# Kernel optimization log

Measured on AMD Instinct MI355X. Metric: run time of the kernel, lower is better.

The kernel has to match this reference:

```python
import jax, jax.numpy as jnp
import numpy as np

N = 131072   # total nodes
E = 262144   # directed edges (avg degree 2, molecular graphs)
G = 4096     # number of graphs in the batch
H = 64       # hidden_dim


def _linear_init(key, fan_in, fan_out):
    # torch.nn.Linear default: U(-1/sqrt(fan_in), 1/sqrt(fan_in))
    s = 1.0 / np.sqrt(fan_in)
    kw, kb = jax.random.split(key)
    W = jax.random.uniform(kw, (fan_in, fan_out), jnp.float32, -s, s)
    b = jax.random.uniform(kb, (fan_out,), jnp.float32, -s, s)
    return W, b


def setup_inputs() -> dict:
    key = jax.random.key(0)
    ks = jax.random.split(key, 8)
    d = {}
    d["x"] = jax.random.normal(ks[0], (N, 1), jnp.float32)
    d["edge_index"] = jax.random.randint(ks[1], (2, E), 0, N, jnp.int32)
    d["batch"] = jnp.sort(jax.random.randint(ks[2], (N,), 0, G, jnp.int32))
    d["W1"], d["b1"] = _linear_init(ks[3], 1, H)          # GCNConv(1, 64)
    d["W2"], d["b2"] = _linear_init(ks[4], H, 2 * H)       # GCNConv(64, 128)
    d["W3"], d["b3"] = _linear_init(ks[5], 2 * H, 4 * H)   # GCNConv(128, 256)
    d["fc1_W"], d["fc1_b"] = _linear_init(ks[6], 4 * H, 128)
    d["fc2_W"], d["fc2_b"] = _linear_init(ks[7], 128, 12)
    return d


def gcn_conv(x, W, b, src, dst):
    """PyG GCNConv: D^-1/2 (A + I) D^-1/2 (x W) + b, self-loops added."""
    h = x @ W                                                   # [N, out]
    deg = jax.ops.segment_sum(jnp.ones(E, jnp.float32), dst, num_segments=N) + 1.0
    dinv = jax.lax.rsqrt(deg)                                   # [N]
    coef = dinv[src] * dinv[dst]                                # [E]
    agg = jax.ops.segment_sum(h[src] * coef[:, None], dst, num_segments=N)
    agg = agg + h * (dinv * dinv)[:, None]                      # self-loop term: h_i / deg_i
    return agg + b


def reference(x, edge_index, batch, W1, b1, W2, b2, W3, b3, fc1_W, fc1_b, fc2_W, fc2_b):
    src, dst = edge_index[0], edge_index[1]
    h = jax.nn.relu(gcn_conv(x, W1, b1, src, dst))
    h = jax.nn.relu(gcn_conv(h, W2, b2, src, dst))
    h = gcn_conv(h, W3, b3, src, dst)                            # [N, 256]
    # global_mean_pool over batch ids
    sums = jax.ops.segment_sum(h, batch, num_segments=G)         # [G, 256]
    cnts = jax.ops.segment_sum(jnp.ones(N, jnp.float32), batch, num_segments=G)
    g = sums / jnp.maximum(cnts, 1.0)[:, None]
    g = jax.nn.relu(g @ fc1_W + fc1_b)
    return g @ fc2_W + fc2_b                                     # [G, 12]
```

## Files before the change

kernel.cpp:

```cpp
#include <hip/hip_runtime.h>

#define NN 131072
#define EE 262144
#define GG 4096

__global__ void k_count(const int* __restrict__ dst, int* __restrict__ indeg) {
    int e = blockIdx.x * 256 + threadIdx.x;
    if (e < EE) atomicAdd(&indeg[dst[e]], 1);
}

__global__ __launch_bounds__(256) void k_scan_a(const int* __restrict__ indeg,
                                                int* __restrict__ bsum,
                                                float* __restrict__ dinv) {
    __shared__ int red[256];
    int tid = threadIdx.x;
    int gid = blockIdx.x * 256 + tid;
    int v = indeg[gid];
    dinv[gid] = rsqrtf((float)v + 1.0f);
    red[tid] = v;
    __syncthreads();
#pragma unroll
    for (int off = 128; off > 0; off >>= 1) {
        if (tid < off) red[tid] += red[tid + off];
        __syncthreads();
    }
    if (tid == 0) bsum[blockIdx.x] = red[0];
}

__global__ __launch_bounds__(512) void k_scan_b(const int* __restrict__ bsum,
                                                int* __restrict__ boff) {
    __shared__ int ps[512];
    int tid = threadIdx.x;
    ps[tid] = bsum[tid];
    __syncthreads();
    for (int off = 1; off < 512; off <<= 1) {
        int v = (tid >= off) ? ps[tid - off] : 0;
        __syncthreads();
        ps[tid] += v;
        __syncthreads();
    }
    boff[tid] = (tid > 0) ? ps[tid - 1] : 0;
    if (tid == 511) boff[512] = ps[511];
}

__global__ __launch_bounds__(256) void k_scan_c(const int* __restrict__ indeg,
                                                const int* __restrict__ boff,
                                                int* __restrict__ rowptr,
                                                int* __restrict__ cursor) {
    __shared__ int ps[256];
    int tid = threadIdx.x;
    int gid = blockIdx.x * 256 + tid;
    int v = indeg[gid];
    ps[tid] = v;
    __syncthreads();
    for (int off = 1; off < 256; off <<= 1) {
        int t = (tid >= off) ? ps[tid - off] : 0;
        __syncthreads();
        ps[tid] += t;
        __syncthreads();
    }
    int excl = boff[blockIdx.x] + ps[tid] - v;
    rowptr[gid] = excl;
    cursor[gid] = excl;
    if (gid == NN - 1) rowptr[NN] = boff[512];
}

__global__ void k_fill_edges(const int* __restrict__ src, const int* __restrict__ dst,
                             const float* __restrict__ dinv,
                             int* __restrict__ cursor, int* __restrict__ ecol,
                             float* __restrict__ ecoef) {
    int e = blockIdx.x * 256 + threadIdx.x;
    if (e < EE) {
        int d = dst[e], s = src[e];
        int slot = atomicAdd(&cursor[d], 1);
        ecol[slot] = s;
        ecoef[slot] = dinv[d] * dinv[s];
    }
}

__global__ void k_z(const float* __restrict__ x, const float* __restrict__ dinv,
                    const int* __restrict__ rowptr, const int* __restrict__ ecol,
                    const float* __restrict__ ecoef, float* __restrict__ z) {
    int i = blockIdx.x * 256 + threadIdx.x;
    if (i < NN) {
        float di = dinv[i];
        float s = x[i] * di * di;
        int e0 = rowptr[i], e1 = rowptr[i + 1];
        for (int e = e0; e < e1; ++e) s += ecoef[e] * x[ecol[e]];
        z[i] = s;
    }
}

__global__ __launch_bounds__(256) void k_gemm2u(const float* __restrict__ z,
                                                const float* __restrict__ dinv,
                                                const int* __restrict__ rowptr,
                                                const int* __restrict__ ecol,
                                                const float* __restrict__ ecoef,
                                                const float* __restrict__ W1,
                                                const float* __restrict__ b1,
                                                const float* __restrict__ W2,
                                                const float* __restrict__ b2,
                                                float* __restrict__ r) {
    __shared__ float At[64][68];
    __shared__ float Wt[64][128];
    __shared__ float w1s[64], b1s[64];

    int tid = threadIdx.x;
    int i0 = blockIdx.x * 64;

    if (tid < 64) { w1s[tid] = W1[tid]; b1s[tid] = b1[tid]; }
    {
        int c4 = tid & 31, kk0 = tid >> 5;
#pragma unroll
        for (int p = 0; p < 8; ++p) {
            int kk = kk0 + p * 8;
            *(float4*)&Wt[kk][c4 * 4] = *(const float4*)&W2[(size_t)kk * 128 + c4 * 4];
        }
    }
    __syncthreads();

    {
        int n = tid >> 2;
        int k0 = (tid & 3) * 16;
        int i = i0 + n;
        float zi = z[i], di = dinv[i];
        float d2 = di * di;
        float uacc[16];
#pragma unroll
        for (int j = 0; j < 16; ++j)
            uacc[j] = d2 * fmaxf(zi * w1s[k0 + j] + b1s[k0 + j], 0.f);
        int e0 = rowptr[i], e1 = rowptr[i + 1];
        for (int e = e0; e < e1; ++e) {
            float w = ecoef[e];
            float zs = z[ecol[e]];
#pragma unroll
            for (int j = 0; j < 16; ++j)
                uacc[j] += w * fmaxf(zs * w1s[k0 + j] + b1s[k0 + j], 0.f);
        }
#pragma unroll
        for (int j = 0; j < 16; ++j) At[n][k0 + j] = uacc[j];
    }
    __syncthreads();

    int colg = tid & 15;
    int rowg = tid >> 4;
    float acc[4][8];
#pragma unroll
    for (int rr = 0; rr < 4; ++rr)
#pragma unroll
        for (int c = 0; c < 8; ++c) acc[rr][c] = 0.0f;

#pragma unroll 4
    for (int kk = 0; kk < 64; ++kk) {
        float a[4];
#pragma unroll
        for (int rr = 0; rr < 4; ++rr) a[rr] = At[rowg * 4 + rr][kk];
        const float4 w0 = *(const float4*)&Wt[kk][colg * 4];
        const float4 w1 = *(const float4*)&Wt[kk][64 + colg * 4];
        float w[8] = {w0.x, w0.y, w0.z, w0.w, w1.x, w1.y, w1.z, w1.w};
#pragma unroll
        for (int rr = 0; rr < 4; ++rr)
#pragma unroll
            for (int c = 0; c < 8; ++c) acc[rr][c] += a[rr] * w[c];
    }

#pragma unroll
    for (int rr = 0; rr < 4; ++rr) {
        int i = i0 + rowg * 4 + rr;
#pragma unroll
        for (int h = 0; h < 2; ++h) {
            int j = h * 64 + colg * 4;
            const float4 b = *(const float4*)&b2[j];
            float4 v;
            v.x = fmaxf(acc[rr][h * 4 + 0] + b.x, 0.f);
            v.y = fmaxf(acc[rr][h * 4 + 1] + b.y, 0.f);
            v.z = fmaxf(acc[rr][h * 4 + 2] + b.z, 0.f);
            v.w = fmaxf(acc[rr][h * 4 + 3] + b.w, 0.f);
            *(float4*)&r[(size_t)i * 128 + j] = v;
        }
    }
}

template <int K, int OUTW, bool RELU_OUT, bool GUARD>
__global__ __launch_bounds__(256) void k_gemm(const float* __restrict__ A,
                                              const float* __restrict__ W,
                                              const float* __restrict__ bias,
                                              const float* __restrict__ cntf,
                                              float* __restrict__ C) {
    __shared__ float At[64][68];
    __shared__ float Wt[64][128];

    int tid  = threadIdx.x;
    int colg = tid & 15;
    int rowg = tid >> 4;
    int i0 = blockIdx.x * 64;
    int j0 = blockIdx.y * 128;

    float acc[4][8];
#pragma unroll
    for (int r = 0; r < 4; ++r)
#pragma unroll
        for (int c = 0; c < 8; ++c) acc[r][c] = 0.0f;

    for (int k0 = 0; k0 < K; k0 += 64) {
        __syncthreads();
        {
            int k4 = tid & 15, r0 = tid >> 4;
#pragma unroll
            for (int p = 0; p < 4; ++p) {
                int r = r0 + p * 16;
                *(float4*)&At[r][k4 * 4] =
                    *(const float4*)&A[(size_t)(i0 + r) * K + k0 + k4 * 4];
            }
        }
        {
            int c4 = tid & 31, kk0 = tid >> 5;
#pragma unroll
            for (int p = 0; p < 8; ++p) {
                int kk = kk0 + p * 8;
                *(float4*)&Wt[kk][c4 * 4] =
                    *(const float4*)&W[(size_t)(k0 + kk) * OUTW + j0 + c4 * 4];
            }
        }
        __syncthreads();
#pragma unroll 4
        for (int kk = 0; kk < 64; ++kk) {
            float a[4];
#pragma unroll
            for (int r = 0; r < 4; ++r) a[r] = At[rowg * 4 + r][kk];
            const float4 w0 = *(const float4*)&Wt[kk][colg * 4];
            const float4 w1 = *(const float4*)&Wt[kk][64 + colg * 4];
            float w[8] = {w0.x, w0.y, w0.z, w0.w, w1.x, w1.y, w1.z, w1.w};
#pragma unroll
            for (int r = 0; r < 4; ++r)
#pragma unroll
                for (int c = 0; c < 8; ++c) acc[r][c] += a[r] * w[c];
        }
    }

#pragma unroll
    for (int r = 0; r < 4; ++r) {
        int i = i0 + rowg * 4 + r;
        float flag = 1.0f;
        if (GUARD) flag = (cntf[i] > 0.0f) ? 1.0f : 0.0f;
#pragma unroll
        for (int h = 0; h < 2; ++h) {
            int j = j0 + h * 64 + colg * 4;
            const float4 b = *(const float4*)&bias[j];
            float4 v;
            v.x = acc[r][h * 4 + 0] + b.x * flag;
            v.y = acc[r][h * 4 + 1] + b.y * flag;
            v.z = acc[r][h * 4 + 2] + b.z * flag;
            v.w = acc[r][h * 4 + 3] + b.w * flag;
            if (RELU_OUT) {
                v.x = fmaxf(v.x, 0.f); v.y = fmaxf(v.y, 0.f);
                v.z = fmaxf(v.z, 0.f); v.w = fmaxf(v.w, 0.f);
            }
            *(float4*)&C[(size_t)i * OUTW + j] = v;
        }
    }
}

__global__ __launch_bounds__(256) void k_fc12(const float* __restrict__ A,
                                              const float* __restrict__ W,
                                              const float* __restrict__ bias,
                                              const float* __restrict__ fc2W,
                                              const float* __restrict__ fc2b,
                                              float* __restrict__ out) {
    __shared__ float At[64][68];
    __shared__ float Wt[64][128];

    int tid  = threadIdx.x;
    int colg = tid & 15;
    int rowg = tid >> 4;
    int i0 = blockIdx.x * 64;

    float acc[4][8];
#pragma unroll
    for (int r = 0; r < 4; ++r)
#pragma unroll
        for (int c = 0; c < 8; ++c) acc[r][c] = 0.0f;

    for (int k0 = 0; k0 < 256; k0 += 64) {
        __syncthreads();
        {
            int k4 = tid & 15, r0 = tid >> 4;
#pragma unroll
            for (int p = 0; p < 4; ++p) {
                int r = r0 + p * 16;
                *(float4*)&At[r][k4 * 4] =
                    *(const float4*)&A[(size_t)(i0 + r) * 256 + k0 + k4 * 4];
            }
        }
        {
            int c4 = tid & 31, kk0 = tid >> 5;
#pragma unroll
            for (int p = 0; p < 8; ++p) {
                int kk = kk0 + p * 8;
                *(float4*)&Wt[kk][c4 * 4] =
                    *(const float4*)&W[(size_t)(k0 + kk) * 128 + c4 * 4];
            }
        }
        __syncthreads();
#pragma unroll 4
        for (int kk = 0; kk < 64; ++kk) {
            float a[4];
#pragma unroll
            for (int r = 0; r < 4; ++r) a[r] = At[rowg * 4 + r][kk];
            const float4 w0 = *(const float4*)&Wt[kk][colg * 4];
            const float4 w1 = *(const float4*)&Wt[kk][64 + colg * 4];
            float w[8] = {w0.x, w0.y, w0.z, w0.w, w1.x, w1.y, w1.z, w1.w};
#pragma unroll
            for (int r = 0; r < 4; ++r)
#pragma unroll
                for (int c = 0; c < 8; ++c) acc[r][c] += a[r] * w[c];
        }
    }
    __syncthreads();
    float* g1s = &Wt[0][0];
    float* w2s = &At[0][0];
    for (int idx = tid; idx < 128 * 12; idx += 256) w2s[idx] = fc2W[idx];

#pragma unroll
    for (int r = 0; r < 4; ++r) {
        int row = rowg * 4 + r;
#pragma unroll
        for (int h = 0; h < 2; ++h) {
            int j = h * 64 + colg * 4;
            const float4 b = *(const float4*)&bias[j];
            float4 v;
            v.x = fmaxf(acc[r][h * 4 + 0] + b.x, 0.f);
            v.y = fmaxf(acc[r][h * 4 + 1] + b.y, 0.f);
            v.z = fmaxf(acc[r][h * 4 + 2] + b.z, 0.f);
            v.w = fmaxf(acc[r][h * 4 + 3] + b.w, 0.f);
            *(float4*)&g1s[row * 128 + j] = v;
        }
    }
    __syncthreads();
    for (int idx = tid; idx < 64 * 12; idx += 256) {
        int row = idx / 12, col = idx % 12;
        float o = fc2b[col];
        const float* gr = &g1s[row * 128];
        for (int k = 0; k < 128; ++k) o += gr[k] * w2s[k * 12 + col];
        out[(size_t)(i0 + row) * 12 + col] = o;
    }
}

__global__ __launch_bounds__(256) void k_pool(const float* __restrict__ r,
                                              const float* __restrict__ dinv,
                                              const int* __restrict__ rowptr,
                                              const int* __restrict__ ecol,
                                              const float* __restrict__ ecoef,
                                              const int* __restrict__ batch,
                                              float* __restrict__ Y,
                                              float* __restrict__ cntf) {
    int g = blockIdx.x, tid = threadIdx.x;
    int l = 0, rr = NN;
    while (l < rr) { int m = (l + rr) >> 1; if (batch[m] < g) l = m + 1; else rr = m; }
    int lo = l;
    rr = NN;
    while (l < rr) { int m = (l + rr) >> 1; if (batch[m] < g + 1) l = m + 1; else rr = m; }
    int hi = l;
    int cnt = hi - lo;

    int lane = tid & 31, ty = tid >> 5;
    int c = lane * 4;
    float4 acc = {0.f, 0.f, 0.f, 0.f};

    int i = lo + ty;
    for (; i + 8 < hi; i += 16) {
        float d0 = dinv[i], d1 = dinv[i + 8];
        const float4 v0 = *(const float4*)&r[(size_t)i * 128 + c];
        const float4 v1 = *(const float4*)&r[(size_t)(i + 8) * 128 + c];
        float w0 = d0 * d0, w1 = d1 * d1;
        acc.x += v0.x * w0 + v1.x * w1;
        acc.y += v0.y * w0 + v1.y * w1;
        acc.z += v0.z * w0 + v1.z * w1;
        acc.w += v0.w * w0 + v1.w * w1;
    }
    for (; i < hi; i += 8) {
        float di = dinv[i], d2 = di * di;
        const float4 v = *(const float4*)&r[(size_t)i * 128 + c];
        acc.x += v.x * d2; acc.y += v.y * d2; acc.z += v.z * d2; acc.w += v.w * d2;
    }

    int e0 = rowptr[lo], e1 = rowptr[hi];
    int e = e0 + ty;
    for (; e + 24 < e1; e += 32) {
        int s0 = ecol[e], s1 = ecol[e + 8], s2 = ecol[e + 16], s3 = ecol[e + 24];
        float w0 = ecoef[e], w1 = ecoef[e + 8], w2 = ecoef[e + 16], w3 = ecoef[e + 24];
        const float4 v0 = *(const float4*)&r[(size_t)s0 * 128 + c];
        const float4 v1 = *(const float4*)&r[(size_t)s1 * 128 + c];
        const float4 v2 = *(const float4*)&r[(size_t)s2 * 128 + c];
        const float4 v3 = *(const float4*)&r[(size_t)s3 * 128 + c];
        acc.x += v0.x * w0 + v1.x * w1 + v2.x * w2 + v3.x * w3;
        acc.y += v0.y * w0 + v1.y * w1 + v2.y * w2 + v3.y * w3;
        acc.z += v0.z * w0 + v1.z * w1 + v2.z * w2 + v3.z * w3;
        acc.w += v0.w * w0 + v1.w * w1 + v2.w * w2 + v3.w * w3;
    }
    for (; e < e1; e += 8) {
        int s = ecol[e];
        float w = ecoef[e];
        const float4 v = *(const float4*)&r[(size_t)s * 128 + c];
        acc.x += v.x * w; acc.y += v.y * w; acc.z += v.z * w; acc.w += v.w * w;
    }

    __shared__ float red[8][128];
    *(float4*)&red[ty][c] = acc;
    __syncthreads();
    if (tid < 128) {
        float s = 0.0f;
#pragma unroll
        for (int t = 0; t < 8; ++t) s += red[t][tid];
        float inv = (cnt > 0) ? 1.0f / (float)cnt : 0.0f;
        Y[(size_t)g * 128 + tid] = s * inv;
    }
    if (tid == 0) cntf[g] = (float)cnt;
}

extern "C" void kernel_launch(void* const* d_in, const int* in_sizes, int n_in,
                              void* d_out, int out_size, void* d_ws, size_t ws_size,
                              hipStream_t stream) {
    const float* x     = (const float*)d_in[0];
    const int*   ei    = (const int*)d_in[1];
    const int*   batch = (const int*)d_in[2];
    const float* W1    = (const float*)d_in[3];
    const float* b1    = (const float*)d_in[4];
    const float* W2    = (const float*)d_in[5];
    const float* b2    = (const float*)d_in[6];
    const float* W3    = (const float*)d_in[7];
    const float* b3    = (const float*)d_in[8];
    const float* fc1W  = (const float*)d_in[9];
    const float* fc1b  = (const float*)d_in[10];
    const float* fc2W  = (const float*)d_in[11];
    const float* fc2b  = (const float*)d_in[12];
    float* out = (float*)d_out;

    const int* srcp = ei;
    const int* dstp = ei + EE;

    float* r      = (float*)d_ws;
    float* Y      = r + (size_t)NN * 128;
    float* pooled = Y + (size_t)GG * 128;
    float* cntf   = pooled + (size_t)GG * 256;
    float* dinv   = cntf + GG;
    float* zbuf   = dinv + NN;
    float* ecoef  = zbuf + NN;
    int* indeg  = (int*)(ecoef + EE);
    int* rowptr = indeg + NN;
    int* cursor = rowptr + NN + 4;
    int* ecol   = cursor + NN;
    int* bsum   = ecol + EE;
    int* boff   = bsum + 512;

    hipMemsetAsync(indeg, 0, NN * sizeof(int), stream);
    k_count<<<EE / 256, 256, 0, stream>>>(dstp, indeg);
    k_scan_a<<<NN / 256, 256, 0, stream>>>(indeg, bsum, dinv);
    k_scan_b<<<1, 512, 0, stream>>>(bsum, boff);
    k_scan_c<<<NN / 256, 256, 0, stream>>>(indeg, boff, rowptr, cursor);
    k_fill_edges<<<EE / 256, 256, 0, stream>>>(srcp, dstp, dinv, cursor, ecol, ecoef);

    k_z<<<NN / 256, 256, 0, stream>>>(x, dinv, rowptr, ecol, ecoef, zbuf);

    k_gemm2u<<<NN / 64, 256, 0, stream>>>(zbuf, dinv, rowptr, ecol, ecoef,
                                          W1, b1, W2, b2, r);

    k_pool<<<GG, 256, 0, stream>>>(r, dinv, rowptr, ecol, ecoef, batch, Y, cntf);

    k_gemm<128, 256, false, true><<<dim3(GG / 64, 2), 256, 0, stream>>>(
        Y, W3, b3, cntf, pooled);
    k_fc12<<<GG / 64, 256, 0, stream>>>(pooled, fc1W, fc1b, fc2W, fc2b, out);
}
```

Before: 158.1 us.

## Fuse head GEMMs, precompute graph starts, shrink gemm2u shared memory

```diff
diff --git a/kernel.cpp b/kernel.cpp
--- a/kernel.cpp
+++ b/kernel.cpp
@@ -11,13 +11,22 @@
 
 __global__ __launch_bounds__(256) void k_scan_a(const int* __restrict__ indeg,
                                                 int* __restrict__ bsum,
-                                                float* __restrict__ dinv) {
+                                                float* __restrict__ dinv,
+                                                const int* __restrict__ batch,
+                                                int* __restrict__ gstart) {
     __shared__ int red[256];
     int tid = threadIdx.x;
     int gid = blockIdx.x * 256 + tid;
     int v = indeg[gid];
     dinv[gid] = rsqrtf((float)v + 1.0f);
     red[tid] = v;
+    {
+        int b1v = batch[gid];
+        int b0v = (gid == 0) ? -1 : batch[gid - 1];
+        for (int g = b0v + 1; g <= b1v; ++g) gstart[g] = gid;
+        if (gid == NN - 1)
+            for (int g = b1v + 1; g <= GG; ++g) gstart[g] = NN;
+    }
     __syncthreads();
 #pragma unroll
     for (int off = 128; off > 0; off >>= 1) {
@@ -101,22 +110,14 @@
                                                 const float* __restrict__ W2,
                                                 const float* __restrict__ b2,
                                                 float* __restrict__ r) {
-    __shared__ float At[64][68];
-    __shared__ float Wt[64][128];
+    __shared__ float At[64][65];
+    __shared__ float Wt[32][128];
     __shared__ float w1s[64], b1s[64];
 
     int tid = threadIdx.x;
     int i0 = blockIdx.x * 64;
 
     if (tid < 64) { w1s[tid] = W1[tid]; b1s[tid] = b1[tid]; }
-    {
-        int c4 = tid & 31, kk0 = tid >> 5;
-#pragma unroll
-        for (int p = 0; p < 8; ++p) {
-            int kk = kk0 + p * 8;
-            *(float4*)&Wt[kk][c4 * 4] = *(const float4*)&W2[(size_t)kk * 128 + c4 * 4];
-        }
-    }
     __syncthreads();
 
     {
@@ -140,7 +141,6 @@
 #pragma unroll
         for (int j = 0; j < 16; ++j) At[n][k0 + j] = uacc[j];
     }
-    __syncthreads();
 
     int colg = tid & 15;
     int rowg = tid >> 4;
@@ -150,18 +150,31 @@
 #pragma unroll
         for (int c = 0; c < 8; ++c) acc[rr][c] = 0.0f;
 
+    for (int kc = 0; kc < 2; ++kc) {
+        if (kc) __syncthreads();
+        {
+            int c4 = tid & 31, kk0 = tid >> 5;
+#pragma unroll
+            for (int p = 0; p < 4; ++p) {
+                int kk = kk0 + p * 8;
+                *(float4*)&Wt[kk][c4 * 4] =
+                    *(const float4*)&W2[(size_t)(kc * 32 + kk) * 128 + c4 * 4];
+            }
+        }
+        __syncthreads();
 #pragma unroll 4
-    for (int kk = 0; kk < 64; ++kk) {
-        float a[4];
-#pragma unroll
-        for (int rr = 0; rr < 4; ++rr) a[rr] = At[rowg * 4 + rr][kk];
-        const float4 w0 = *(const float4*)&Wt[kk][colg * 4];
-        const float4 w1 = *(const float4*)&Wt[kk][64 + colg * 4];
-        float w[8] = {w0.x, w0.y, w0.z, w0.w, w1.x, w1.y, w1.z, w1.w};
-#pragma unroll
-        for (int rr = 0; rr < 4; ++rr)
-#pragma unroll
-            for (int c = 0; c < 8; ++c) acc[rr][c] += a[rr] * w[c];
+        for (int kk = 0; kk < 32; ++kk) {
+            float a[4];
+#pragma unroll
+            for (int rr = 0; rr < 4; ++rr) a[rr] = At[rowg * 4 + rr][kc * 32 + kk];
+            const float4 w0 = *(const float4*)&Wt[kk][colg * 4];
+            const float4 w1 = *(const float4*)&Wt[kk][64 + colg * 4];
+            float w[8] = {w0.x, w0.y, w0.z, w0.w, w1.x, w1.y, w1.z, w1.w};
+#pragma unroll
+            for (int rr = 0; rr < 4; ++rr)
+#pragma unroll
+                for (int c = 0; c < 8; ++c) acc[rr][c] += a[rr] * w[c];
+        }
     }
 
 #pragma unroll
@@ -181,186 +194,16 @@
     }
 }
 
-template <int K, int OUTW, bool RELU_OUT, bool GUARD>
-__global__ __launch_bounds__(256) void k_gemm(const float* __restrict__ A,
-                                              const float* __restrict__ W,
-                                              const float* __restrict__ bias,
-                                              const float* __restrict__ cntf,
-                                              float* __restrict__ C) {
-    __shared__ float At[64][68];
-    __shared__ float Wt[64][128];
-
-    int tid  = threadIdx.x;
-    int colg = tid & 15;
-    int rowg = tid >> 4;
-    int i0 = blockIdx.x * 64;
-    int j0 = blockIdx.y * 128;
-
-    float acc[4][8];
-#pragma unroll
-    for (int r = 0; r < 4; ++r)
-#pragma unroll
-        for (int c = 0; c < 8; ++c) acc[r][c] = 0.0f;
-
-    for (int k0 = 0; k0 < K; k0 += 64) {
-        __syncthreads();
-        {
-            int k4 = tid & 15, r0 = tid >> 4;
-#pragma unroll
-            for (int p = 0; p < 4; ++p) {
-                int r = r0 + p * 16;
-                *(float4*)&At[r][k4 * 4] =
-                    *(const float4*)&A[(size_t)(i0 + r) * K + k0 + k4 * 4];
-            }
-        }
-        {
-            int c4 = tid & 31, kk0 = tid >> 5;
-#pragma unroll
-            for (int p = 0; p < 8; ++p) {
-                int kk = kk0 + p * 8;
-                *(float4*)&Wt[kk][c4 * 4] =
-                    *(const float4*)&W[(size_t)(k0 + kk) * OUTW + j0 + c4 * 4];
-            }
-        }
-        __syncthreads();
-#pragma unroll 4
-        for (int kk = 0; kk < 64; ++kk) {
-            float a[4];
-#pragma unroll
-            for (int r = 0; r < 4; ++r) a[r] = At[rowg * 4 + r][kk];
-            const float4 w0 = *(const float4*)&Wt[kk][colg * 4];
-            const float4 w1 = *(const float4*)&Wt[kk][64 + colg * 4];
-            float w[8] = {w0.x, w0.y, w0.z, w0.w, w1.x, w1.y, w1.z, w1.w};
-#pragma unroll
-            for (int r = 0; r < 4; ++r)
-#pragma unroll
-                for (int c = 0; c < 8; ++c) acc[r][c] += a[r] * w[c];
-        }
-    }
-
-#pragma unroll
-    for (int r = 0; r < 4; ++r) {
-        int i = i0 + rowg * 4 + r;
-        float flag = 1.0f;
-        if (GUARD) flag = (cntf[i] > 0.0f) ? 1.0f : 0.0f;
-#pragma unroll
-        for (int h = 0; h < 2; ++h) {
-            int j = j0 + h * 64 + colg * 4;
-            const float4 b = *(const float4*)&bias[j];
-            float4 v;
-            v.x = acc[r][h * 4 + 0] + b.x * flag;
-            v.y = acc[r][h * 4 + 1] + b.y * flag;
-            v.z = acc[r][h * 4 + 2] + b.z * flag;
-            v.w = acc[r][h * 4 + 3] + b.w * flag;
-            if (RELU_OUT) {
-                v.x = fmaxf(v.x, 0.f); v.y = fmaxf(v.y, 0.f);
-                v.z = fmaxf(v.z, 0.f); v.w = fmaxf(v.w, 0.f);
-            }
-            *(float4*)&C[(size_t)i * OUTW + j] = v;
-        }
-    }
-}
-
-__global__ __launch_bounds__(256) void k_fc12(const float* __restrict__ A,
-                                              const float* __restrict__ W,
-                                              const float* __restrict__ bias,
-                                              const float* __restrict__ fc2W,
-                                              const float* __restrict__ fc2b,
-                                              float* __restrict__ out) {
-    __shared__ float At[64][68];
-    __shared__ float Wt[64][128];
-
-    int tid  = threadIdx.x;
-    int colg = tid & 15;
-    int rowg = tid >> 4;
-    int i0 = blockIdx.x * 64;
-
-    float acc[4][8];
-#pragma unroll
-    for (int r = 0; r < 4; ++r)
-#pragma unroll
-        for (int c = 0; c < 8; ++c) acc[r][c] = 0.0f;
-
-    for (int k0 = 0; k0 < 256; k0 += 64) {
-        __syncthreads();
-        {
-            int k4 = tid & 15, r0 = tid >> 4;
-#pragma unroll
-            for (int p = 0; p < 4; ++p) {
-                int r = r0 + p * 16;
-                *(float4*)&At[r][k4 * 4] =
-                    *(const float4*)&A[(size_t)(i0 + r) * 256 + k0 + k4 * 4];
-            }
-        }
-        {
-            int c4 = tid & 31, kk0 = tid >> 5;
-#pragma unroll
-            for (int p = 0; p < 8; ++p) {
-                int kk = kk0 + p * 8;
-                *(float4*)&Wt[kk][c4 * 4] =
-                    *(const float4*)&W[(size_t)(k0 + kk) * 128 + c4 * 4];
-            }
-        }
-        __syncthreads();
-#pragma unroll 4
-        for (int kk = 0; kk < 64; ++kk) {
-            float a[4];
-#pragma unroll
-            for (int r = 0; r < 4; ++r) a[r] = At[rowg * 4 + r][kk];
-            const float4 w0 = *(const float4*)&Wt[kk][colg * 4];
-            const float4 w1 = *(const float4*)&Wt[kk][64 + colg * 4];
-            float w[8] = {w0.x, w0.y, w0.z, w0.w, w1.x, w1.y, w1.z, w1.w};
-#pragma unroll
-            for (int r = 0; r < 4; ++r)
-#pragma unroll
-                for (int c = 0; c < 8; ++c) acc[r][c] += a[r] * w[c];
-        }
-    }
-    __syncthreads();
-    float* g1s = &Wt[0][0];
-    float* w2s = &At[0][0];
-    for (int idx = tid; idx < 128 * 12; idx += 256) w2s[idx] = fc2W[idx];
-
-#pragma unroll
-    for (int r = 0; r < 4; ++r) {
-        int row = rowg * 4 + r;
-#pragma unroll
-        for (int h = 0; h < 2; ++h) {
-            int j = h * 64 + colg * 4;
-            const float4 b = *(const float4*)&bias[j];
-            float4 v;
-            v.x = fmaxf(acc[r][h * 4 + 0] + b.x, 0.f);
-            v.y = fmaxf(acc[r][h * 4 + 1] + b.y, 0.f);
-            v.z = fmaxf(acc[r][h * 4 + 2] + b.z, 0.f);
-            v.w = fmaxf(acc[r][h * 4 + 3] + b.w, 0.f);
-            *(float4*)&g1s[row * 128 + j] = v;
-        }
-    }
-    __syncthreads();
-    for (int idx = tid; idx < 64 * 12; idx += 256) {
-        int row = idx / 12, col = idx % 12;
-        float o = fc2b[col];
-        const float* gr = &g1s[row * 128];
-        for (int k = 0; k < 128; ++k) o += gr[k] * w2s[k * 12 + col];
-        out[(size_t)(i0 + row) * 12 + col] = o;
-    }
-}
-
 __global__ __launch_bounds__(256) void k_pool(const float* __restrict__ r,
                                               const float* __restrict__ dinv,
                                               const int* __restrict__ rowptr,
                                               const int* __restrict__ ecol,
                                               const float* __restrict__ ecoef,
-                                              const int* __restrict__ batch,
+                                              const int* __restrict__ gstart,
                                               float* __restrict__ Y,
                                               float* __restrict__ cntf) {
     int g = blockIdx.x, tid = threadIdx.x;
-    int l = 0, rr = NN;
-    while (l < rr) { int m = (l + rr) >> 1; if (batch[m] < g) l = m + 1; else rr = m; }
-    int lo = l;
-    rr = NN;
-    while (l < rr) { int m = (l + rr) >> 1; if (batch[m] < g + 1) l = m + 1; else rr = m; }
-    int hi = l;
+    int lo = gstart[g], hi = gstart[g + 1];
     int cnt = hi - lo;
 
     int lane = tid & 31, ty = tid >> 5;
@@ -416,6 +259,146 @@
         Y[(size_t)g * 128 + tid] = s * inv;
     }
     if (tid == 0) cntf[g] = (float)cnt;
+}
+
+__global__ __launch_bounds__(256) void k_head3(const float* __restrict__ Y,
+                                               const float* __restrict__ cntf,
+                                               const float* __restrict__ W3,
+                                               const float* __restrict__ b3,
+                                               const float* __restrict__ fc1W,
+                                               const float* __restrict__ fc1b,
+                                               const float* __restrict__ fc2W,
+                                               const float* __restrict__ fc2b,
+                                               float* __restrict__ out) {
+    __shared__ float At[64][68];
+    __shared__ float Wt[64][128];
+    __shared__ float pS[64][260];
+
+    int tid  = threadIdx.x;
+    int colg = tid & 15;
+    int rowg = tid >> 4;
+    int i0 = blockIdx.x * 64;
+
+    for (int jh = 0; jh < 2; ++jh) {
+        float acc[4][8];
+#pragma unroll
+        for (int rr = 0; rr < 4; ++rr)
+#pragma unroll
+            for (int c = 0; c < 8; ++c) acc[rr][c] = 0.0f;
+
+        for (int k0 = 0; k0 < 128; k0 += 64) {
+            __syncthreads();
+            {
+                int k4 = tid & 15, r0 = tid >> 4;
+#pragma unroll
+                for (int p = 0; p < 4; ++p) {
+                    int rr = r0 + p * 16;
+                    *(float4*)&At[rr][k4 * 4] =
+                        *(const float4*)&Y[(size_t)(i0 + rr) * 128 + k0 + k4 * 4];
+                }
+            }
+            {
+                int c4 = tid & 31, kk0 = tid >> 5;
+#pragma unroll
+                for (int p = 0; p < 8; ++p) {
+                    int kk = kk0 + p * 8;
+                    *(float4*)&Wt[kk][c4 * 4] =
+                        *(const float4*)&W3[(size_t)(k0 + kk) * 256 + jh * 128 + c4 * 4];
+                }
+            }
+            __syncthreads();
+#pragma unroll 4
+            for (int kk = 0; kk < 64; ++kk) {
+                float a[4];
+#pragma unroll
+                for (int rr = 0; rr < 4; ++rr) a[rr] = At[rowg * 4 + rr][kk];
+                const float4 w0 = *(const float4*)&Wt[kk][colg * 4];
+                const float4 w1 = *(const float4*)&Wt[kk][64 + colg * 4];
+                float w[8] = {w0.x, w0.y, w0.z, w0.w, w1.x, w1.y, w1.z, w1.w};
+#pragma unroll
+                for (int rr = 0; rr < 4; ++rr)
+#pragma unroll
+                    for (int c = 0; c < 8; ++c) acc[rr][c] += a[rr] * w[c];
+            }
+        }
+#pragma unroll
+        for (int rr = 0; rr < 4; ++rr) {
+            int row = rowg * 4 + rr;
+            float flag = (cntf[i0 + row] > 0.0f) ? 1.0f : 0.0f;
+#pragma unroll
+            for (int h = 0; h < 2; ++h) {
+                int j = jh * 128 + h * 64 + colg * 4;
+                const float4 b = *(const float4*)&b3[j];
+                pS[row][j + 0] = acc[rr][h * 4 + 0] + b.x * flag;
+                pS[row][j + 1] = acc[rr][h * 4 + 1] + b.y * flag;
+                pS[row][j + 2] = acc[rr][h * 4 + 2] + b.z * flag;
+                pS[row][j + 3] = acc[rr][h * 4 + 3] + b.w * flag;
+            }
+        }
+    }
+    __syncthreads();
+
+    float acc[4][8];
+#pragma unroll
+    for (int rr = 0; rr < 4; ++rr)
+#pragma unroll
+        for (int c = 0; c < 8; ++c) acc[rr][c] = 0.0f;
+
+    for (int k0 = 0; k0 < 256; k0 += 64) {
+        if (k0) __syncthreads();
+        {
+            int c4 = tid & 31, kk0 = tid >> 5;
+#pragma unroll
+            for (int p = 0; p < 8; ++p) {
+                int kk = kk0 + p * 8;
+                *(float4*)&Wt[kk][c4 * 4] =
+                    *(const float4*)&fc1W[(size_t)(k0 + kk) * 128 + c4 * 4];
+            }
+        }
+        __syncthreads();
+#pragma unroll 4
+        for (int kk = 0; kk < 64; ++kk) {
+            float a[4];
+#pragma unroll
+            for (int rr = 0; rr < 4; ++rr) a[rr] = pS[rowg * 4 + rr][k0 + kk];
+            const float4 w0 = *(const float4*)&Wt[kk][colg * 4];
+            const float4 w1 = *(const float4*)&Wt[kk][64 + colg * 4];
+            float w[8] = {w0.x, w0.y, w0.z, w0.w, w1.x, w1.y, w1.z, w1.w};
+#pragma unroll
+            for (int rr = 0; rr < 4; ++rr)
+#pragma unroll
+                for (int c = 0; c < 8; ++c) acc[rr][c] += a[rr] * w[c];
+        }
+    }
+    __syncthreads();
+
+    float* g1s = &Wt[0][0];
+    float* w2s = &At[0][0];
+#pragma unroll
+    for (int rr = 0; rr < 4; ++rr) {
+        int row = rowg * 4 + rr;
+#pragma unroll
+        for (int h = 0; h < 2; ++h) {
+            int j = h * 64 + colg * 4;
+            const float4 b = *(const float4*)&fc1b[j];
+            float4 v;
+            v.x = fmaxf(acc[rr][h * 4 + 0] + b.x, 0.f);
+            v.y = fmaxf(acc[rr][h * 4 + 1] + b.y, 0.f);
+            v.z = fmaxf(acc[rr][h * 4 + 2] + b.z, 0.f);
+            v.w = fmaxf(acc[rr][h * 4 + 3] + b.w, 0.f);
+            *(float4*)&g1s[row * 128 + j] = v;
+        }
+    }
+    for (int idx = tid; idx < 128 * 12; idx += 256) w2s[idx] = fc2W[idx];
+    __syncthreads();
+
+    for (int idx = tid; idx < 64 * 12; idx += 256) {
+        int row = idx / 12, col = idx % 12;
+        float o = fc2b[col];
+        const float* gr = &g1s[row * 128];
+        for (int k = 0; k < 128; ++k) o += gr[k] * w2s[k * 12 + col];
+        out[(size_t)(i0 + row) * 12 + col] = o;
+    }
 }
 
 extern "C" void kernel_launch(void* const* d_in, const int* in_sizes, int n_in,
@@ -441,8 +424,7 @@
 
     float* r      = (float*)d_ws;
     float* Y      = r + (size_t)NN * 128;
-    float* pooled = Y + (size_t)GG * 128;
-    float* cntf   = pooled + (size_t)GG * 256;
+    float* cntf   = Y + (size_t)GG * 128;
     float* dinv   = cntf + GG;
     float* zbuf   = dinv + NN;
     float* ecoef  = zbuf + NN;
@@ -452,10 +434,11 @@
     int* ecol   = cursor + NN;
     int* bsum   = ecol + EE;
     int* boff   = bsum + 512;
+    int* gstart = boff + 516;
 
     hipMemsetAsync(indeg, 0, NN * sizeof(int), stream);
     k_count<<<EE / 256, 256, 0, stream>>>(dstp, indeg);
-    k_scan_a<<<NN / 256, 256, 0, stream>>>(indeg, bsum, dinv);
+    k_scan_a<<<NN / 256, 256, 0, stream>>>(indeg, bsum, dinv, batch, gstart);
     k_scan_b<<<1, 512, 0, stream>>>(bsum, boff);
     k_scan_c<<<NN / 256, 256, 0, stream>>>(indeg, boff, rowptr, cursor);
     k_fill_edges<<<EE / 256, 256, 0, stream>>>(srcp, dstp, dinv, cursor, ecol, ecoef);
@@ -465,9 +448,8 @@
     k_gemm2u<<<NN / 64, 256, 0, stream>>>(zbuf, dinv, rowptr, ecol, ecoef,
                                           W1, b1, W2, b2, r);
 
-    k_pool<<<GG, 256, 0, stream>>>(r, dinv, rowptr, ecol, ecoef, batch, Y, cntf);
-
-    k_gemm<128, 256, false, true><<<dim3(GG / 64, 2), 256, 0, stream>>>(
-        Y, W3, b3, cntf, pooled);
-    k_fc12<<<GG / 64, 256, 0, stream>>>(pooled, fc1W, fc1b, fc2W, fc2b, out);
-}
+    k_pool<<<GG, 256, 0, stream>>>(r, dinv, rowptr, ecol, ecoef, gstart, Y, cntf);
+
+    k_head3<<<GG / 64, 256, 0, stream>>>(Y, cntf, W3, b3, fc1W, fc1b,
+                                         fc2W, fc2b, out);
+}
```

Measured after the change: 155.6 us. About the same (-1.6%).

## Precompute graph segment starts and shrink gemm2u shared memory footprint

Applied to the files above, without the earlier changes.

```diff
diff --git a/kernel.cpp b/kernel.cpp
--- a/kernel.cpp
+++ b/kernel.cpp
@@ -11,13 +11,22 @@
 
 __global__ __launch_bounds__(256) void k_scan_a(const int* __restrict__ indeg,
                                                 int* __restrict__ bsum,
-                                                float* __restrict__ dinv) {
+                                                float* __restrict__ dinv,
+                                                const int* __restrict__ batch,
+                                                int* __restrict__ gstart) {
     __shared__ int red[256];
     int tid = threadIdx.x;
     int gid = blockIdx.x * 256 + tid;
     int v = indeg[gid];
     dinv[gid] = rsqrtf((float)v + 1.0f);
     red[tid] = v;
+    {
+        int b1v = batch[gid];
+        int b0v = (gid == 0) ? -1 : batch[gid - 1];
+        for (int g = b0v + 1; g <= b1v; ++g) gstart[g] = gid;
+        if (gid == NN - 1)
+            for (int g = b1v + 1; g <= GG; ++g) gstart[g] = NN;
+    }
     __syncthreads();
 #pragma unroll
     for (int off = 128; off > 0; off >>= 1) {
@@ -101,22 +110,14 @@
                                                 const float* __restrict__ W2,
                                                 const float* __restrict__ b2,
                                                 float* __restrict__ r) {
-    __shared__ float At[64][68];
-    __shared__ float Wt[64][128];
+    __shared__ float At[64][65];
+    __shared__ float Wt[32][128];
     __shared__ float w1s[64], b1s[64];
 
     int tid = threadIdx.x;
     int i0 = blockIdx.x * 64;
 
     if (tid < 64) { w1s[tid] = W1[tid]; b1s[tid] = b1[tid]; }
-    {
-        int c4 = tid & 31, kk0 = tid >> 5;
-#pragma unroll
-        for (int p = 0; p < 8; ++p) {
-            int kk = kk0 + p * 8;
-            *(float4*)&Wt[kk][c4 * 4] = *(const float4*)&W2[(size_t)kk * 128 + c4 * 4];
-        }
-    }
     __syncthreads();
 
     {
@@ -140,7 +141,6 @@
 #pragma unroll
         for (int j = 0; j < 16; ++j) At[n][k0 + j] = uacc[j];
     }
-    __syncthreads();
 
     int colg = tid & 15;
     int rowg = tid >> 4;
@@ -150,18 +150,31 @@
 #pragma unroll
         for (int c = 0; c < 8; ++c) acc[rr][c] = 0.0f;
 
+    for (int kc = 0; kc < 2; ++kc) {
+        if (kc) __syncthreads();
+        {
+            int c4 = tid & 31, kk0 = tid >> 5;
+#pragma unroll
+            for (int p = 0; p < 4; ++p) {
+                int kk = kk0 + p * 8;
+                *(float4*)&Wt[kk][c4 * 4] =
+                    *(const float4*)&W2[(size_t)(kc * 32 + kk) * 128 + c4 * 4];
+            }
+        }
+        __syncthreads();
 #pragma unroll 4
-    for (int kk = 0; kk < 64; ++kk) {
-        float a[4];
-#pragma unroll
-        for (int rr = 0; rr < 4; ++rr) a[rr] = At[rowg * 4 + rr][kk];
-        const float4 w0 = *(const float4*)&Wt[kk][colg * 4];
-        const float4 w1 = *(const float4*)&Wt[kk][64 + colg * 4];
-        float w[8] = {w0.x, w0.y, w0.z, w0.w, w1.x, w1.y, w1.z, w1.w};
-#pragma unroll
-        for (int rr = 0; rr < 4; ++rr)
-#pragma unroll
-            for (int c = 0; c < 8; ++c) acc[rr][c] += a[rr] * w[c];
+        for (int kk = 0; kk < 32; ++kk) {
+            float a[4];
+#pragma unroll
+            for (int rr = 0; rr < 4; ++rr) a[rr] = At[rowg * 4 + rr][kc * 32 + kk];
+            const float4 w0 = *(const float4*)&Wt[kk][colg * 4];
+            const float4 w1 = *(const float4*)&Wt[kk][64 + colg * 4];
+            float w[8] = {w0.x, w0.y, w0.z, w0.w, w1.x, w1.y, w1.z, w1.w};
+#pragma unroll
+            for (int rr = 0; rr < 4; ++rr)
+#pragma unroll
+                for (int c = 0; c < 8; ++c) acc[rr][c] += a[rr] * w[c];
+        }
     }
 
 #pragma unroll
@@ -351,16 +364,11 @@
                                               const int* __restrict__ rowptr,
                                               const int* __restrict__ ecol,
                                               const float* __restrict__ ecoef,
-                                              const int* __restrict__ batch,
+                                              const int* __restrict__ gstart,
                                               float* __restrict__ Y,
                                               float* __restrict__ cntf) {
     int g = blockIdx.x, tid = threadIdx.x;
-    int l = 0, rr = NN;
-    while (l < rr) { int m = (l + rr) >> 1; if (batch[m] < g) l = m + 1; else rr = m; }
-    int lo = l;
-    rr = NN;
-    while (l < rr) { int m = (l + rr) >> 1; if (batch[m] < g + 1) l = m + 1; else rr = m; }
-    int hi = l;
+    int lo = gstart[g], hi = gstart[g + 1];
     int cnt = hi - lo;
 
     int lane = tid & 31, ty = tid >> 5;
@@ -452,10 +460,11 @@
     int* ecol   = cursor + NN;
     int* bsum   = ecol + EE;
     int* boff   = bsum + 512;
+    int* gstart = boff + 516;
 
     hipMemsetAsync(indeg, 0, NN * sizeof(int), stream);
     k_count<<<EE / 256, 256, 0, stream>>>(dstp, indeg);
-    k_scan_a<<<NN / 256, 256, 0, stream>>>(indeg, bsum, dinv);
+    k_scan_a<<<NN / 256, 256, 0, stream>>>(indeg, bsum, dinv, batch, gstart);
     k_scan_b<<<1, 512, 0, stream>>>(bsum, boff);
     k_scan_c<<<NN / 256, 256, 0, stream>>>(indeg, boff, rowptr, cursor);
     k_fill_edges<<<EE / 256, 256, 0, stream>>>(srcp, dstp, dinv, cursor, ecol, ecoef);
@@ -465,7 +474,7 @@
     k_gemm2u<<<NN / 64, 256, 0, stream>>>(zbuf, dinv, rowptr, ecol, ecoef,
                                           W1, b1, W2, b2, r);
 
-    k_pool<<<GG, 256, 0, stream>>>(r, dinv, rowptr, ecol, ecoef, batch, Y, cntf);
+    k_pool<<<GG, 256, 0, stream>>>(r, dinv, rowptr, ecol, ecoef, gstart, Y, cntf);
 
     k_gemm<128, 256, false, true><<<dim3(GG / 64, 2), 256, 0, stream>>>(
         Y, W3, b3, cntf, pooled);
```

Result: faster. 148.6 us (-6.0%).
